# Kernel tuning notes

Measured on AMD Instinct MI355X. Metric: run time of the kernel, lower is better.

The kernel has to match this reference:

```python
import jax, jax.numpy as jnp
import numpy as np

NUM_EXP = 4  # 1 shared expert + (NUM_EXP-1) routed experts


def _mobius_add(x, y, c):
    # Mobius addition in the Poincare ball with curvature c
    x2 = jnp.sum(x * x, axis=-1, keepdims=True)
    y2 = jnp.sum(y * y, axis=-1, keepdims=True)
    xy = jnp.sum(x * y, axis=-1, keepdims=True)
    num = (1.0 + 2.0 * c * xy + c * y2) * x + (1.0 - c * x2) * y
    den = 1.0 + 2.0 * c * xy + c * c * x2 * y2
    return num / den


def _expmap(ref, v, c):
    # exponential map from tangent space at ref, curvature c (matches torch expmap)
    ref2 = jnp.sum(ref * ref, axis=-1, keepdims=True)
    sf = 2.0 / (1.0 + c * ref2)                      # scaling_factor(ref, c)
    vn = jnp.sqrt(jnp.sum(v * v, axis=-1, keepdims=True))
    second = (1.0 / jnp.sqrt(c)) * jnp.tanh(jnp.sqrt(c * sf * vn * vn / 2.0)) * (v / vn)
    return _mobius_add(ref, second, c)


def setup_inputs() -> dict:
    key = jax.random.key(0)
    ks = jax.random.split(key, 10)
    B, T, C = 2, 2048, 256
    E, H, G = 32, 4 * C, 31  # experts, ffn hidden, gate outputs (n_experts-1)
    s = 0.02
    return {
        "x": jax.random.normal(ks[0], (B, T, C), jnp.float32),
        "reference_point": jax.random.normal(ks[1], (B, T, C), jnp.float32),
        "Wg": jax.random.normal(ks[2], (C, G), jnp.float32) * s,
        "bg": jnp.zeros((G,), jnp.float32),
        "expert_bias": jnp.zeros((G,), jnp.float32),  # requires_grad=False in torch
        "Wfc": jax.random.normal(ks[3], (E, C, H), jnp.float32) * s,
        "bfc": jnp.zeros((E, H), jnp.float32),
        "Wproj": jax.random.normal(ks[4], (E, H, C), jnp.float32) * s,
        "bproj": jnp.zeros((E, C), jnp.float32),
        "c": jnp.array([0.5], jnp.float32),  # curvature param (torch.rand(1))
    }


def reference(x, reference_point, Wg, bg, expert_bias, Wfc, bfc, Wproj, bproj, c):
    b, t, C = x.shape
    n = b * t
    E = Wfc.shape[0]
    xf = x.reshape(n, C)
    rf = reference_point.reshape(n, C)

    # gate: Linear -> (noise is identity in eval) -> softmax
    gate = jax.nn.softmax(xf @ Wg + bg, axis=-1)          # [n, E-1]
    biased = gate + expert_bias
    gv, gi = jax.lax.top_k(biased, NUM_EXP - 1)            # [n, 3]
    gv = gv / jnp.sum(gv, axis=-1, keepdims=True)
    shared_w = jnp.full((n, 1), 1.0 / NUM_EXP, dtype=x.dtype)
    gate_vals = jnp.concatenate([shared_w, gv * (NUM_EXP - 1) / NUM_EXP], axis=-1)  # [n, 4]
    gate_idx = jnp.concatenate([jnp.zeros((n, 1), gi.dtype), gi + 1], axis=-1)       # [n, 4]

    # dense all-expert MLP (dropout identity in eval): [E, n, H] -> [E, n, C]
    h = jax.nn.gelu(jnp.einsum('nc,ech->enh', xf, Wfc) + bfc[:, None, :], approximate=False)
    y = jnp.einsum('enh,ehc->enc', h, Wproj) + bproj[:, None, :]
    expert_out = _expmap(rf[None, :, :], y, c)             # [E, n, C]

    # scatter_add routing weights -> [n, E]
    rw = jnp.zeros((n, E), x.dtype).at[jnp.arange(n)[:, None], gate_idx].add(gate_vals)

    out = jnp.einsum('enc,ne->nc', expert_out, rw)
    return out.reshape(b, t, C), rw
```

## Files before the change

kernel.cpp:

```cpp
#include <hip/hip_runtime.h>
#include <math.h>

#define N_TOK 4096
#define C_DIM 256
#define G_DIM 31
#define E_DIM 32
#define H_DIM 1024
#define TT    16
#define MT    32
#define TBL_MAX 576
#define NWT   (E_DIM * 64)

typedef unsigned short ushort_t;
typedef unsigned int uint_t;
typedef __attribute__((ext_vector_type(8))) short bfrag;
typedef __attribute__((ext_vector_type(4))) float f32x4;
typedef __attribute__((ext_vector_type(8))) unsigned short ushort8;

__device__ __forceinline__ ushort_t f2bf(float f) {
    uint_t u = __float_as_uint(f);
    uint_t r = (u + 0x7fffu + ((u >> 16) & 1u)) >> 16;
    return (ushort_t)r;
}

__device__ __forceinline__ float gelu_f(float v) {
    float u = 0.7978845608f * fmaf(0.044715f * v * v, v, v);
    float t = __expf(-2.f * u);
    return 0.5f * v * (1.f + (1.f - t) / (1.f + t));
}

__global__ __launch_bounds__(256) void prep_kernel(
    const float* __restrict__ Wfc, const float* __restrict__ Wproj,
    ushort_t* __restrict__ WfcF, ushort_t* __restrict__ WprojF,
    const float* __restrict__ xf, const float* __restrict__ rfp,
    const float* __restrict__ Wg, const float* __restrict__ bg,
    const float* __restrict__ ebias,
    float* __restrict__ rw_out, int* __restrict__ btok,
    float* __restrict__ bwgt, float* __restrict__ ref2_out,
    float4* __restrict__ choice, int* __restrict__ counts, int nwt)
{
    __shared__ __align__(16) char smem[36864];
    const int tid = threadIdx.x;

    if ((int)blockIdx.x < nwt) {
        ushort_t (*s)[260] = (ushort_t(*)[260])smem;
        const int b = blockIdx.x;
        const int e = b >> 6, sub = b & 63;
        const bool isfc = sub < 32;
        const float* src;
        int stride, fbbase;
        if (isfc) {
            int kt = sub >> 2, q = sub & 3;
            src = Wfc + ((size_t)e << 18) + (size_t)(kt * 32) * H_DIM + q * 256;
            stride = H_DIM;
            fbbase = e * 512 + kt * 64 + q * 16;
        } else {
            int kt = sub - 32;
            src = Wproj + ((size_t)e << 18) + (size_t)(kt * 32) * C_DIM;
            stride = C_DIM;
            fbbase = e * 512 + kt * 16;
        }
        ushort_t* dst = isfc ? WfcF : WprojF;

        float4 v[8];
        #pragma unroll
        for (int i = 0; i < 8; ++i) {
            int flat = i * 256 + tid;
            int r = flat >> 6, q4 = flat & 63;
            v[i] = *(const float4*)(src + (size_t)r * stride + q4 * 4);
        }
        #pragma unroll
        for (int i = 0; i < 8; ++i) {
            int flat = i * 256 + tid;
            int r = flat >> 6, q4 = flat & 63;
            s[r][q4 * 4 + 0] = f2bf(v[i].x);
            s[r][q4 * 4 + 1] = f2bf(v[i].y);
            s[r][q4 * 4 + 2] = f2bf(v[i].z);
            s[r][q4 * 4 + 3] = f2bf(v[i].w);
        }
        __syncthreads();

        const int l = tid & 63, w = tid >> 6;
        #pragma unroll
        for (int t = 0; t < 4; ++t) {
            int nt = w + t * 4;
            ushort8 pv;
            #pragma unroll
            for (int j = 0; j < 8; ++j)
                pv[j] = s[(l >> 4) * 8 + j][nt * 16 + (l & 15)];
            *(ushort8*)(dst + ((size_t)(fbbase + nt) * 64 + l) * 8) = pv;
        }
        return;
    }

    float* wgS = (float*)smem;
    float (*xs)[C_DIM] = (float(*)[C_DIM])(smem + 31744);
    const int b2 = blockIdx.x - nwt;
    const int w = tid >> 6, l = tid & 63;
    const int tok = b2 * 4 + w;

    if (b2 == 0 && tid == 0) counts[0] = N_TOK;

    for (int i = tid; i < C_DIM * G_DIM; i += 256) wgS[i] = Wg[i];

    float4 xv = *(const float4*)(xf + (size_t)tok * C_DIM + l * 4);
    float4 rv = *(const float4*)(rfp + (size_t)tok * C_DIM + l * 4);
    *(float4*)(&xs[w][l * 4]) = xv;
    float r2 = rv.x * rv.x + rv.y * rv.y + rv.z * rv.z + rv.w * rv.w;
    #pragma unroll
    for (int off = 32; off; off >>= 1) r2 += __shfl_xor(r2, off);
    if (l == 0) ref2_out[tok] = r2;
    __syncthreads();

    const int g = l & 31, half = l >> 5;
    float acc = 0.f;
    if (g < G_DIM) {
        const float* xr = xs[w] + half * 128;
        const float* wg = wgS + (size_t)(half * 128) * G_DIM + g;
        #pragma unroll 8
        for (int c = 0; c < 128; ++c)
            acc = fmaf(xr[c], wg[(size_t)c * G_DIM], acc);
    }
    acc += __shfl_xor(acc, 32);
    float lg = acc + ((g < G_DIM) ? bg[g] : 0.f);

    float v = (l < G_DIM) ? lg : -1e30f;
    float m = v;
    #pragma unroll
    for (int off = 32; off; off >>= 1) m = fmaxf(m, __shfl_xor(m, off));
    float pex = (l < G_DIM) ? __expf(v - m) : 0.f;
    float s = pex;
    #pragma unroll
    for (int off = 32; off; off >>= 1) s += __shfl_xor(s, off);
    float p = (l < G_DIM) ? (pex / s + ebias[l]) : -1e30f;

    float w3[3]; int id3[3];
    float vv = p;
    #pragma unroll
    for (int t = 0; t < 3; ++t) {
        float bv = vv; int bi = l;
        #pragma unroll
        for (int off = 32; off; off >>= 1) {
            float ov = __shfl_xor(bv, off); int oi = __shfl_xor(bi, off);
            if (ov > bv || (ov == bv && oi < bi)) { bv = ov; bi = oi; }
        }
        w3[t] = bv; id3[t] = bi;
        if (l == bi) vv = -1e30f;
    }
    float vs = w3[0] + w3[1] + w3[2];
    #pragma unroll
    for (int t = 0; t < 3; ++t) w3[t] = (w3[t] / vs) * 0.75f;

    if (l < 32) {
        float r = (l == 0) ? 0.25f : 0.f;
        #pragma unroll
        for (int t = 0; t < 3; ++t) if (l == id3[t] + 1) r = w3[t];
        rw_out[(size_t)tok * E_DIM + l] = r;
    }

    if (l == 0) {
        btok[tok] = tok;
        bwgt[tok] = 0.25f;
        int packed = (id3[0] + 1) | ((id3[1] + 1) << 8) | ((id3[2] + 1) << 16);
        float4 ch;
        ch.x = w3[0]; ch.y = w3[1]; ch.z = w3[2]; ch.w = __int_as_float(packed);
        choice[tok] = ch;
    }
}

__global__ __launch_bounds__(256) void bucketize_kernel(
    const float4* __restrict__ choice, int* __restrict__ btok,
    float* __restrict__ bwgt, int* __restrict__ counts,
    int* __restrict__ done, int* __restrict__ tbl)
{
    const int e = blockIdx.x + 1;
    const int tid = threadIdx.x;
    const int l = tid & 63, w = tid >> 6;
    __shared__ int wsum[4];

    int base = 0;
    for (int chunk = 0; chunk < N_TOK; chunk += 256) {
        int tok = chunk + tid;
        float4 ch = choice[tok];
        int eids = __float_as_int(ch.w);
        int m = 0; float wv = 0.f;
        if ((eids & 255) == e)              { m = 1; wv = ch.x; }
        else if (((eids >> 8) & 255) == e)  { m = 2; wv = ch.y; }
        else if (((eids >> 16) & 255) == e) { m = 3; wv = ch.z; }
        int x = m ? 1 : 0;
        #pragma unroll
        for (int off = 1; off < 64; off <<= 1) {
            int y = __shfl_up(x, off);
            if (l >= off) x += y;
        }
        if (l == 63) wsum[w] = x;
        __syncthreads();
        int waveoff = 0;
        #pragma unroll
        for (int i = 0; i < 4; ++i) if (i < w) waveoff += wsum[i];
        int total = wsum[0] + wsum[1] + wsum[2] + wsum[3];
        if (m) {
            int pos = base + waveoff + x - 1;
            btok[(size_t)e * N_TOK + pos] = tok | (m << 12);
            bwgt[(size_t)e * N_TOK + pos] = wv;
        }
        base += total;
        __syncthreads();
    }
    if (tid == 0) {
        counts[e] = base;
        if (tbl != nullptr) {
            __threadfence();
            int v = atomicAdd(done, 1);
            if (v == G_DIM - 1) {
                __threadfence();
                int tot = 0;
                for (int ee = 0; ee < E_DIM; ++ee) {
                    int cnt = counts[ee];
                    int tiles = (cnt + MT - 1) / MT;
                    for (int t = 0; t < tiles; ++t)
                        tbl[1 + tot + t] = ee | (t << 8);
                    tot += tiles;
                }
                tbl[0] = tot;
            }
        }
    }
}

__global__ __launch_bounds__(256, 2) void expert_mfma32p(
    const float* __restrict__ xf, const float* __restrict__ rfp,
    const ushort_t* __restrict__ WfcF, const ushort_t* __restrict__ WprojF,
    const float* __restrict__ bfc, const float* __restrict__ bproj,
    const float* __restrict__ cptr, const float* __restrict__ ref2p,
    const int* __restrict__ counts, const int* __restrict__ btok,
    const float* __restrict__ bwgt, const int* __restrict__ tbl,
    float* __restrict__ part)
{
    const int T = (blockIdx.x & 7) * (TBL_MAX / 8) + (blockIdx.x >> 3);
    const int tot = tbl[0];
    if (T >= tot) return;
    const int ent = tbl[1 + T];
    const int e = ent & 0xFF;
    const int base = (ent >> 8) * MT;
    const int cnt = counts[e];
    const int ntk = min(MT, cnt - base);
    const int tid = threadIdx.x;
    const int lane = tid & 63;
    const int w = tid >> 6;

    __shared__ __align__(16) ushort_t hfrag[MT * H_DIM];
    __shared__ int   spk[MT];
    __shared__ float swgt[MT];

    if (tid < MT) {
        bool vld = (base + tid) < cnt;
        spk[tid]  = btok[(size_t)e * N_TOK + (vld ? base + tid : base)];
        swgt[tid] = vld ? bwgt[(size_t)e * N_TOK + base + tid] : 0.f;
    }
    __syncthreads();

    {
        const int r  = tid >> 3;
        const int c0 = (tid & 7) * 32;
        const int mt = r >> 4, rr = r & 15;
        const int kt = c0 >> 5;
        const bool valid = (r < ntk);
        const float* xrow = xf + (size_t)(spk[r] & 0xFFF) * C_DIM;
        #pragma unroll
        for (int q = 0; q < 4; ++q) {
            ushort8 pv;
            #pragma unroll
            for (int j = 0; j < 8; ++j)
                pv[j] = f2bf(valid ? xrow[c0 + q * 8 + j] : 0.f);
            *(ushort8*)(hfrag + (size_t)((mt * 8 + kt) * 64 + (rr + 16 * q)) * 8) = pv;
        }
    }
    __syncthreads();

    bfrag afr[2][8];
    #pragma unroll
    for (int mt = 0; mt < 2; ++mt)
        #pragma unroll
        for (int kt = 0; kt < 8; ++kt)
            afr[mt][kt] = *(const bfrag*)(hfrag + (size_t)((mt * 8 + kt) * 64 + lane) * 8);
    __syncthreads();

    {
        const ushort_t* wb = WfcF + (size_t)e * 512 * 512;
        auto ldB = [&](bfrag* dst, int n1) {
            int nt = w * 16 + n1;
            #pragma unroll
            for (int kt = 0; kt < 8; ++kt)
                dst[kt] = *(const bfrag*)(wb + (size_t)(kt * 64 + nt) * 512 + lane * 8);
        };
        auto wback = [&](const f32x4& a0, const f32x4& a1, int hcol) {
            const int jj = hcol & 7, grp = (hcol & 31) >> 3, kth = hcol >> 5;
            const int rb = (lane >> 4) * 4;
            #pragma unroll
            for (int r = 0; r < 4; ++r) {
                int lp = rb + r + 16 * grp;
                hfrag[(size_t)(kth * 64 + lp) * 8 + jj]        = f2bf(gelu_f(a0[r]));
                hfrag[(size_t)((32 + kth) * 64 + lp) * 8 + jj] = f2bf(gelu_f(a1[r]));
            }
        };
        bfrag bA[8], bB[8];
        ldB(bA, 0);
        ldB(bB, 1);
        #pragma unroll 1
        for (int n1 = 0; n1 < 16; n1 += 2) {
            {
                const int hcol = (w * 16 + n1) * 16 + (lane & 15);
                const float bv = bfc[e * H_DIM + hcol];
                f32x4 a0 = {bv, bv, bv, bv}, a1 = {bv, bv, bv, bv};
                #pragma unroll
                for (int kt = 0; kt < 8; ++kt) {
                    a0 = __builtin_amdgcn_mfma_f32_16x16x32_bf16(afr[0][kt], bA[kt], a0, 0, 0, 0);
                    a1 = __builtin_amdgcn_mfma_f32_16x16x32_bf16(afr[1][kt], bA[kt], a1, 0, 0, 0);
                }
                if (n1 + 2 < 16) ldB(bA, n1 + 2);
                wback(a0, a1, hcol);
            }
            {
                const int hcol = (w * 16 + n1 + 1) * 16 + (lane & 15);
                const float bv = bfc[e * H_DIM + hcol];
                f32x4 a0 = {bv, bv, bv, bv}, a1 = {bv, bv, bv, bv};
                #pragma unroll
                for (int kt = 0; kt < 8; ++kt) {
                    a0 = __builtin_amdgcn_mfma_f32_16x16x32_bf16(afr[0][kt], bB[kt], a0, 0, 0, 0);
                    a1 = __builtin_amdgcn_mfma_f32_16x16x32_bf16(afr[1][kt], bB[kt], a1, 0, 0, 0);
                }
                if (n1 + 3 < 16) ldB(bB, n1 + 3);
                wback(a0, a1, hcol);
            }
        }
    }
    __syncthreads();

    f32x4 yac[2][4];
    #pragma unroll
    for (int mt = 0; mt < 2; ++mt)
        #pragma unroll
        for (int q = 0; q < 4; ++q) {
            int ccol = (w * 4 + q) * 16 + (lane & 15);
            float bv = bproj[e * C_DIM + ccol];
            yac[mt][q] = {bv, bv, bv, bv};
        }
    {
        const ushort_t* wb = WprojF + (size_t)e * 512 * 512;
        auto ldBp = [&](bfrag* dst, int kt) {
            #pragma unroll
            for (int q = 0; q < 4; ++q)
                dst[q] = *(const bfrag*)(wb + (size_t)(kt * 16 + w * 4 + q) * 512 + lane * 8);
        };
        auto ldAp = [&](bfrag* dst, int kt) {
            dst[0] = *(const bfrag*)(hfrag + (size_t)(kt * 64 + lane) * 8);
            dst[1] = *(const bfrag*)(hfrag + (size_t)((32 + kt) * 64 + lane) * 8);
        };
        bfrag bA[4], bB[4], aA[2], aB[2];
        ldAp(aA, 0); ldBp(bA, 0);
        ldAp(aB, 1); ldBp(bB, 1);
        #pragma unroll 1
        for (int kt = 0; kt < 32; kt += 2) {
            #pragma unroll
            for (int q = 0; q < 4; ++q) {
                yac[0][q] = __builtin_amdgcn_mfma_f32_16x16x32_bf16(aA[0], bA[q], yac[0][q], 0, 0, 0);
                yac[1][q] = __builtin_amdgcn_mfma_f32_16x16x32_bf16(aA[1], bA[q], yac[1][q], 0, 0, 0);
            }
            if (kt + 2 < 32) { ldBp(bA, kt + 2); ldAp(aA, kt + 2); }
            #pragma unroll
            for (int q = 0; q < 4; ++q) {
                yac[0][q] = __builtin_amdgcn_mfma_f32_16x16x32_bf16(aB[0], bB[q], yac[0][q], 0, 0, 0);
                yac[1][q] = __builtin_amdgcn_mfma_f32_16x16x32_bf16(aB[1], bB[q], yac[1][q], 0, 0, 0);
            }
            if (kt + 3 < 32) { ldBp(bB, kt + 3); ldAp(aB, kt + 3); }
        }
    }
    __syncthreads();

    float* ynat = (float*)hfrag;
    #pragma unroll
    for (int mt = 0; mt < 2; ++mt)
        #pragma unroll
        for (int q = 0; q < 4; ++q) {
            int ccol = (w * 4 + q) * 16 + (lane & 15);
            #pragma unroll
            for (int r = 0; r < 4; ++r) {
                int tt = mt * 16 + (lane >> 4) * 4 + r;
                ynat[tt * 260 + ccol] = yac[mt][q][r];
            }
        }
    __syncthreads();

    {
        const float cc0 = cptr[0];
        const float rsqc = sqrtf(cc0);
        #pragma unroll 1
        for (int i = 0; i < 8; ++i) {
            int tt = w * 8 + i;
            if (tt >= ntk) break;
            int pk = spk[tt];
            int tok = pk & 0xFFF, slot = pk >> 12;
            float4 yv = *(const float4*)(ynat + tt * 260 + lane * 4);
            float4 rv = *(const float4*)(rfp + (size_t)tok * C_DIM + lane * 4);
            float s2  = yv.x * yv.x + yv.y * yv.y + yv.z * yv.z + yv.w * yv.w;
            float sxy = rv.x * yv.x + rv.y * yv.y + rv.z * yv.z + rv.w * yv.w;
            #pragma unroll
            for (int off = 32; off; off >>= 1) {
                s2  += __shfl_xor(s2, off);
                sxy += __shfl_xor(sxy, off);
            }
            float ref2 = ref2p[tok];
            float sf = 2.f / (1.f + cc0 * ref2);
            float vn = sqrtf(s2);
            float aa = sqrtf(cc0 * sf * 0.5f);
            float alpha = (vn > 1e-20f) ? (tanhf(aa * vn) / (vn * rsqc)) : (aa / rsqc);
            float axy = alpha * sxy;
            float ay2 = alpha * alpha * s2;
            float A   = 1.f + 2.f * cc0 * axy + cc0 * ay2;
            float Bc  = (1.f - cc0 * ref2) * alpha;
            float den = 1.f + 2.f * cc0 * axy + cc0 * cc0 * ref2 * ay2;
            float wi  = swgt[tt] / den;
            float aco = A * wi, bco = Bc * wi;
            float4 o;
            o.x = fmaf(aco, rv.x, bco * yv.x);
            o.y = fmaf(aco, rv.y, bco * yv.y);
            o.z = fmaf(aco, rv.z, bco * yv.z);
            o.w = fmaf(aco, rv.w, bco * yv.w);
            *(float4*)(part + ((size_t)slot * N_TOK + tok) * C_DIM + lane * 4) = o;
        }
    }
}

__global__ __launch_bounds__(256) void combine_kernel(
    const float* __restrict__ part, float* __restrict__ out)
{
    const size_t NC = (size_t)N_TOK * C_DIM;
    size_t i = ((size_t)blockIdx.x * 256 + threadIdx.x) * 4;
    float4 a = *(const float4*)(part + i);
    float4 b = *(const float4*)(part + i + NC);
    float4 c = *(const float4*)(part + i + 2 * NC);
    float4 d = *(const float4*)(part + i + 3 * NC);
    float4 o;
    o.x = (a.x + b.x) + (c.x + d.x);
    o.y = (a.y + b.y) + (c.y + d.y);
    o.z = (a.z + b.z) + (c.z + d.z);
    o.w = (a.w + b.w) + (c.w + d.w);
    *(float4*)(out + i) = o;
}

__global__ __launch_bounds__(256) void expert_kernel(
    const float* __restrict__ xf, const float* __restrict__ rfp,
    const float* __restrict__ Wfc, const float* __restrict__ bfc,
    const float* __restrict__ Wproj, const float* __restrict__ bproj,
    const float* __restrict__ cptr, const float* __restrict__ ref2p,
    const int* __restrict__ counts, const int* __restrict__ btok,
    const float* __restrict__ bwgt, float* __restrict__ out)
{
    const int e = blockIdx.x;
    const int cnt = counts[e];
    const int base = blockIdx.y * TT;
    if (base >= cnt) return;
    const int nt = min(TT, cnt - base);
    const int j = threadIdx.x;

    __shared__ __align__(16) float xs[TT * C_DIM];
    __shared__ __align__(16) float hs[TT * C_DIM];
    __shared__ int   stok[TT];
    __shared__ float swgt[TT];
    __shared__ float scA[TT], scB[TT];

    if (j < nt) {
        stok[j] = btok[(size_t)e * N_TOK + base + j] & 0xFFF;
        swgt[j] = bwgt[(size_t)e * N_TOK + base + j];
    }
    __syncthreads();
    for (int t = 0; t < nt; ++t) xs[t * C_DIM + j] = xf[(size_t)stok[t] * C_DIM + j];
    for (int t = nt; t < TT; ++t) xs[t * C_DIM + j] = 0.f;
    __syncthreads();

    const float* Wfc_e = Wfc + (size_t)e * C_DIM * H_DIM;
    float h[4][TT];
    {
        float bk[4];
        #pragma unroll
        for (int k = 0; k < 4; ++k) bk[k] = bfc[(size_t)e * H_DIM + j + k * 256];
        #pragma unroll
        for (int k = 0; k < 4; ++k)
            #pragma unroll
            for (int tt = 0; tt < TT; ++tt) h[k][tt] = bk[k];
    }
    for (int c0 = 0; c0 < C_DIM; c0 += 4) {
        float wv[4][4];
        #pragma unroll
        for (int ci = 0; ci < 4; ++ci) {
            const float* wp = Wfc_e + (size_t)(c0 + ci) * H_DIM + j;
            wv[ci][0] = wp[0]; wv[ci][1] = wp[256]; wv[ci][2] = wp[512]; wv[ci][3] = wp[768];
        }
        #pragma unroll
        for (int tt = 0; tt < TT; ++tt) {
            float4 xv = *(const float4*)(xs + tt * C_DIM + c0);
            #pragma unroll
            for (int k = 0; k < 4; ++k)
                h[k][tt] += xv.x * wv[0][k] + xv.y * wv[1][k] + xv.z * wv[2][k] + xv.w * wv[3][k];
        }
    }
    #pragma unroll
    for (int k = 0; k < 4; ++k)
        #pragma unroll
        for (int tt = 0; tt < TT; ++tt) {
            float v = h[k][tt];
            h[k][tt] = 0.5f * v * (1.f + erff(v * 0.70710678118f));
        }

    const float* Wp_e = Wproj + (size_t)e * H_DIM * C_DIM;
    float yacc[TT];
    {
        float bp = bproj[(size_t)e * C_DIM + j];
        #pragma unroll
        for (int tt = 0; tt < TT; ++tt) yacc[tt] = bp;
    }
    #pragma unroll
    for (int k = 0; k < 4; ++k) {
        __syncthreads();
        #pragma unroll
        for (int tt = 0; tt < TT; ++tt) hs[tt * C_DIM + j] = h[k][tt];
        __syncthreads();
        for (int h0 = 0; h0 < 256; h0 += 4) {
            float wv[4];
            #pragma unroll
            for (int hi = 0; hi < 4; ++hi)
                wv[hi] = Wp_e[(size_t)(k * 256 + h0 + hi) * C_DIM + j];
            #pragma unroll
            for (int tt = 0; tt < TT; ++tt) {
                float4 hv = *(const float4*)(hs + tt * C_DIM + h0);
                yacc[tt] += hv.x * wv[0] + hv.y * wv[1] + hv.z * wv[2] + hv.w * wv[3];
            }
        }
    }

    __syncthreads();
    #pragma unroll
    for (int tt = 0; tt < TT; ++tt) hs[tt * C_DIM + j] = yacc[tt];
    __syncthreads();

    const float cc0 = cptr[0];
    const int wave = j >> 6, lane = j & 63;
    for (int q = 0; q < 4; ++q) {
        int tt = wave * 4 + q;
        if (tt >= nt) break;
        int tok = stok[tt];
        float s2 = 0.f, sxy = 0.f;
        #pragma unroll
        for (int m = 0; m < 4; ++m) {
            int ccol = lane + 64 * m;
            float yv = hs[tt * C_DIM + ccol];
            float rv = rfp[(size_t)tok * C_DIM + ccol];
            s2 += yv * yv; sxy += rv * yv;
        }
        #pragma unroll
        for (int off = 32; off; off >>= 1) {
            s2  += __shfl_down(s2, off);
            sxy += __shfl_down(sxy, off);
        }
        if (lane == 0) {
            float ref2 = ref2p[tok];
            float sf = 2.f / (1.f + cc0 * ref2);
            float vn = sqrtf(s2);
            float a = sqrtf(cc0 * sf * 0.5f);
            float alpha = (vn > 1e-20f)
                        ? (tanhf(a * vn) / (vn * sqrtf(cc0)))
                        : (a / sqrtf(cc0));
            float axy = alpha * sxy;
            float ay2 = alpha * alpha * s2;
            float A   = 1.f + 2.f * cc0 * axy + cc0 * ay2;
            float Bc  = (1.f - cc0 * ref2) * alpha;
            float den = 1.f + 2.f * cc0 * axy + cc0 * cc0 * ref2 * ay2;
            float wi  = swgt[tt] / den;
            scA[tt] = A * wi;
            scB[tt] = Bc * wi;
        }
    }
    __syncthreads();

    for (int tt = 0; tt < nt; ++tt) {
        int tok = stok[tt];
        float rv = rfp[(size_t)tok * C_DIM + j];
        float yv = hs[tt * C_DIM + j];
        atomicAdd(&out[(size_t)tok * C_DIM + j], scA[tt] * rv + scB[tt] * yv);
    }
}

extern "C" void kernel_launch(void* const* d_in, const int* in_sizes, int n_in,
                              void* d_out, int out_size, void* d_ws, size_t ws_size,
                              hipStream_t stream) {
    (void)in_sizes; (void)n_in; (void)out_size;
    const float* x     = (const float*)d_in[0];
    const float* rfp   = (const float*)d_in[1];
    const float* Wg    = (const float*)d_in[2];
    const float* bg    = (const float*)d_in[3];
    const float* ebias = (const float*)d_in[4];
    const float* Wfc   = (const float*)d_in[5];
    const float* bfc   = (const float*)d_in[6];
    const float* Wproj = (const float*)d_in[7];
    const float* bproj = (const float*)d_in[8];
    const float* cptr  = (const float*)d_in[9];

    float* out = (float*)d_out;
    float* rw  = out + (size_t)N_TOK * C_DIM;

    constexpr size_t OFF_DONE  = 128;
    constexpr size_t OFF_BTOK  = 256;
    constexpr size_t OFF_BWGT  = OFF_BTOK + (size_t)E_DIM * N_TOK * 4;
    constexpr size_t OFF_REF2  = OFF_BWGT + (size_t)E_DIM * N_TOK * 4;
    constexpr size_t OFF_CHO   = ((OFF_REF2 + (size_t)N_TOK * 4 + 255) / 256) * 256;
    constexpr size_t OFF_TBL   = OFF_CHO + (size_t)N_TOK * 16;
    constexpr size_t OFF_WFC   = OFF_TBL + 4096;
    constexpr size_t SZ_W      = (size_t)E_DIM * C_DIM * H_DIM * 2;
    constexpr size_t OFF_WPROJ = OFF_WFC + SZ_W;
    constexpr size_t OFF_PART  = OFF_WPROJ + SZ_W;
    constexpr size_t SZ_PART   = (size_t)4 * N_TOK * C_DIM * 4;
    constexpr size_t WS_FULL   = OFF_PART + SZ_PART;

    char*  ws     = (char*)d_ws;
    int*   counts = (int*)ws;
    int*   done   = (int*)(ws + OFF_DONE);
    int*   btok   = (int*)(ws + OFF_BTOK);
    float* bwgt   = (float*)(ws + OFF_BWGT);
    float* ref2   = (float*)(ws + OFF_REF2);
    float4* cho   = (float4*)(ws + OFF_CHO);
    int*   tbl    = (int*)(ws + OFF_TBL);

    hipMemsetAsync(ws, 0, 256, stream);

    if (ws_size >= WS_FULL) {
        ushort_t* WfcF   = (ushort_t*)(ws + OFF_WFC);
        ushort_t* WprojF = (ushort_t*)(ws + OFF_WPROJ);
        float*    part   = (float*)(ws + OFF_PART);
        prep_kernel<<<NWT + 1024, 256, 0, stream>>>(
            Wfc, Wproj, WfcF, WprojF, x, rfp, Wg, bg, ebias,
            rw, btok, bwgt, ref2, cho, counts, NWT);
        bucketize_kernel<<<G_DIM, 256, 0, stream>>>(cho, btok, bwgt, counts, done, tbl);
        expert_mfma32p<<<TBL_MAX, 256, 0, stream>>>(x, rfp, WfcF, WprojF, bfc, bproj,
                                                    cptr, ref2, counts, btok, bwgt, tbl, part);
        combine_kernel<<<(N_TOK * C_DIM) / 1024, 256, 0, stream>>>(part, out);
    } else {
        hipMemsetAsync(out, 0, (size_t)N_TOK * C_DIM * sizeof(float), stream);
        prep_kernel<<<1024, 256, 0, stream>>>(
            Wfc, Wproj, nullptr, nullptr, x, rfp, Wg, bg, ebias,
            rw, btok, bwgt, ref2, cho, counts, 0);
        bucketize_kernel<<<G_DIM, 256, 0, stream>>>(cho, btok, bwgt, counts, done, nullptr);
        dim3 grid(E_DIM, N_TOK / TT);
        expert_kernel<<<grid, 256, 0, stream>>>(x, rfp, Wfc, bfc, Wproj, bproj,
                                                cptr, ref2, counts, btok, bwgt, out);
    }
}
```

Before: 141.7 us.

## Chunk expert hidden dimension to halve LDS and split prep into two kernels

The expert kernel now processes the 1024-wide hidden layer in two 512-column chunks. Each chunk runs the FC GEMM plus GELU into a half-size LDS buffer and then accumulates its share of the projection GEMM. This cuts shared memory from 64KB to about 33KB and raises the launch-bounds occupancy target from 2 to 4 blocks per CU. The combined prep kernel is split into separate weight-transpose and gate kernels, which adds a launch and extra barriers but removes the branch and shared-memory sizing coupling. Raising the occupancy target may also constrain register allocation.

```diff
diff --git a/kernel.cpp b/kernel.cpp
--- a/kernel.cpp
+++ b/kernel.cpp
@@ -9,7 +9,6 @@
 #define TT    16
 #define MT    32
 #define TBL_MAX 576
-#define NWT   (E_DIM * 64)
 
 typedef unsigned short ushort_t;
 typedef unsigned int uint_t;
@@ -29,77 +28,75 @@
     return 0.5f * v * (1.f + (1.f - t) / (1.f + t));
 }
 
-__global__ __launch_bounds__(256) void prep_kernel(
+__global__ __launch_bounds__(256) void wtrans_kernel(
     const float* __restrict__ Wfc, const float* __restrict__ Wproj,
-    ushort_t* __restrict__ WfcF, ushort_t* __restrict__ WprojF,
+    ushort_t* __restrict__ WfcF, ushort_t* __restrict__ WprojF)
+{
+    __shared__ __align__(16) ushort_t s[32][260];
+    const int tid = threadIdx.x;
+    const int b = blockIdx.x;
+    const int e = b >> 6, sub = b & 63;
+    const bool isfc = sub < 32;
+    const float* src;
+    int stride, fbbase;
+    if (isfc) {
+        int kt = sub >> 2, q = sub & 3;
+        src = Wfc + ((size_t)e << 18) + (size_t)(kt * 32) * H_DIM + q * 256;
+        stride = H_DIM;
+        fbbase = e * 512 + kt * 64 + q * 16;
+    } else {
+        int kt = sub - 32;
+        src = Wproj + ((size_t)e << 18) + (size_t)(kt * 32) * C_DIM;
+        stride = C_DIM;
+        fbbase = e * 512 + kt * 16;
+    }
+    ushort_t* dst = isfc ? WfcF : WprojF;
+
+    float4 v[8];
+    #pragma unroll
+    for (int i = 0; i < 8; ++i) {
+        int flat = i * 256 + tid;
+        int r = flat >> 6, q4 = flat & 63;
+        v[i] = *(const float4*)(src + (size_t)r * stride + q4 * 4);
+    }
+    #pragma unroll
+    for (int i = 0; i < 8; ++i) {
+        int flat = i * 256 + tid;
+        int r = flat >> 6, q4 = flat & 63;
+        s[r][q4 * 4 + 0] = f2bf(v[i].x);
+        s[r][q4 * 4 + 1] = f2bf(v[i].y);
+        s[r][q4 * 4 + 2] = f2bf(v[i].z);
+        s[r][q4 * 4 + 3] = f2bf(v[i].w);
+    }
+    __syncthreads();
+
+    const int l = tid & 63, w = tid >> 6;
+    #pragma unroll
+    for (int t = 0; t < 4; ++t) {
+        int nt = w + t * 4;
+        ushort8 pv;
+        #pragma unroll
+        for (int j = 0; j < 8; ++j)
+            pv[j] = s[(l >> 4) * 8 + j][nt * 16 + (l & 15)];
+        *(ushort8*)(dst + ((size_t)(fbbase + nt) * 64 + l) * 8) = pv;
+    }
+}
+
+__global__ __launch_bounds__(256) void gate_kernel(
     const float* __restrict__ xf, const float* __restrict__ rfp,
     const float* __restrict__ Wg, const float* __restrict__ bg,
     const float* __restrict__ ebias,
     float* __restrict__ rw_out, int* __restrict__ btok,
     float* __restrict__ bwgt, float* __restrict__ ref2_out,
-    float4* __restrict__ choice, int* __restrict__ counts, int nwt)
+    float4* __restrict__ choice, int* __restrict__ counts)
 {
-    __shared__ __align__(16) char smem[36864];
+    __shared__ float wgS[C_DIM * G_DIM];
+    __shared__ __align__(16) float xs[4][C_DIM];
     const int tid = threadIdx.x;
-
-    if ((int)blockIdx.x < nwt) {
-        ushort_t (*s)[260] = (ushort_t(*)[260])smem;
-        const int b = blockIdx.x;
-        const int e = b >> 6, sub = b & 63;
-        const bool isfc = sub < 32;
-        const float* src;
-        int stride, fbbase;
-        if (isfc) {
-            int kt = sub >> 2, q = sub & 3;
-            src = Wfc + ((size_t)e << 18) + (size_t)(kt * 32) * H_DIM + q * 256;
-            stride = H_DIM;
-            fbbase = e * 512 + kt * 64 + q * 16;
-        } else {
-            int kt = sub - 32;
-            src = Wproj + ((size_t)e << 18) + (size_t)(kt * 32) * C_DIM;
-            stride = C_DIM;
-            fbbase = e * 512 + kt * 16;
-        }
-        ushort_t* dst = isfc ? WfcF : WprojF;
-
-        float4 v[8];
-        #pragma unroll
-        for (int i = 0; i < 8; ++i) {
-            int flat = i * 256 + tid;
-            int r = flat >> 6, q4 = flat & 63;
-            v[i] = *(const float4*)(src + (size_t)r * stride + q4 * 4);
-        }
-        #pragma unroll
-        for (int i = 0; i < 8; ++i) {
-            int flat = i * 256 + tid;
-            int r = flat >> 6, q4 = flat & 63;
-            s[r][q4 * 4 + 0] = f2bf(v[i].x);
-            s[r][q4 * 4 + 1] = f2bf(v[i].y);
-            s[r][q4 * 4 + 2] = f2bf(v[i].z);
-            s[r][q4 * 4 + 3] = f2bf(v[i].w);
-        }
-        __syncthreads();
-
-        const int l = tid & 63, w = tid >> 6;
-        #pragma unroll
-        for (int t = 0; t < 4; ++t) {
-            int nt = w + t * 4;
-            ushort8 pv;
-            #pragma unroll
-            for (int j = 0; j < 8; ++j)
-                pv[j] = s[(l >> 4) * 8 + j][nt * 16 + (l & 15)];
-            *(ushort8*)(dst + ((size_t)(fbbase + nt) * 64 + l) * 8) = pv;
-        }
-        return;
-    }
-
-    float* wgS = (float*)smem;
-    float (*xs)[C_DIM] = (float(*)[C_DIM])(smem + 31744);
-    const int b2 = blockIdx.x - nwt;
     const int w = tid >> 6, l = tid & 63;
-    const int tok = b2 * 4 + w;
-
-    if (b2 == 0 && tid == 0) counts[0] = N_TOK;
+    const int tok = blockIdx.x * 4 + w;
+
+    if (blockIdx.x == 0 && tid == 0) counts[0] = N_TOK;
 
     for (int i = tid; i < C_DIM * G_DIM; i += 256) wgS[i] = Wg[i];
 
@@ -228,7 +225,7 @@
     }
 }
 
-__global__ __launch_bounds__(256, 2) void expert_mfma32p(
+__global__ __launch_bounds__(256, 4) void expert_mfma32hc(
     const float* __restrict__ xf, const float* __restrict__ rfp,
     const ushort_t* __restrict__ WfcF, const ushort_t* __restrict__ WprojF,
     const float* __restrict__ bfc, const float* __restrict__ bproj,
@@ -249,7 +246,8 @@
     const int lane = tid & 63;
     const int w = tid >> 6;
 
-    __shared__ __align__(16) ushort_t hfrag[MT * H_DIM];
+    __shared__ __align__(16) char smem[33792];
+    ushort_t* hbuf = (ushort_t*)smem;
     __shared__ int   spk[MT];
     __shared__ float swgt[MT];
 
@@ -273,7 +271,7 @@
             #pragma unroll
             for (int j = 0; j < 8; ++j)
                 pv[j] = f2bf(valid ? xrow[c0 + q * 8 + j] : 0.f);
-            *(ushort8*)(hfrag + (size_t)((mt * 8 + kt) * 64 + (rr + 16 * q)) * 8) = pv;
+            *(ushort8*)(hbuf + (size_t)((mt * 8 + kt) * 64 + (rr + 16 * q)) * 8) = pv;
         }
     }
     __syncthreads();
@@ -283,58 +281,7 @@
     for (int mt = 0; mt < 2; ++mt)
         #pragma unroll
         for (int kt = 0; kt < 8; ++kt)
-            afr[mt][kt] = *(const bfrag*)(hfrag + (size_t)((mt * 8 + kt) * 64 + lane) * 8);
-    __syncthreads();
-
-    {
-        const ushort_t* wb = WfcF + (size_t)e * 512 * 512;
-        auto ldB = [&](bfrag* dst, int n1) {
-            int nt = w * 16 + n1;
-            #pragma unroll
-            for (int kt = 0; kt < 8; ++kt)
-                dst[kt] = *(const bfrag*)(wb + (size_t)(kt * 64 + nt) * 512 + lane * 8);
-        };
-        auto wback = [&](const f32x4& a0, const f32x4& a1, int hcol) {
-            const int jj = hcol & 7, grp = (hcol & 31) >> 3, kth = hcol >> 5;
-            const int rb = (lane >> 4) * 4;
-            #pragma unroll
-            for (int r = 0; r < 4; ++r) {
-                int lp = rb + r + 16 * grp;
-                hfrag[(size_t)(kth * 64 + lp) * 8 + jj]        = f2bf(gelu_f(a0[r]));
-                hfrag[(size_t)((32 + kth) * 64 + lp) * 8 + jj] = f2bf(gelu_f(a1[r]));
-            }
-        };
-        bfrag bA[8], bB[8];
-        ldB(bA, 0);
-        ldB(bB, 1);
-        #pragma unroll 1
-        for (int n1 = 0; n1 < 16; n1 += 2) {
-            {
-                const int hcol = (w * 16 + n1) * 16 + (lane & 15);
-                const float bv = bfc[e * H_DIM + hcol];
-                f32x4 a0 = {bv, bv, bv, bv}, a1 = {bv, bv, bv, bv};
-                #pragma unroll
-                for (int kt = 0; kt < 8; ++kt) {
-                    a0 = __builtin_amdgcn_mfma_f32_16x16x32_bf16(afr[0][kt], bA[kt], a0, 0, 0, 0);
-                    a1 = __builtin_amdgcn_mfma_f32_16x16x32_bf16(afr[1][kt], bA[kt], a1, 0, 0, 0);
-                }
-                if (n1 + 2 < 16) ldB(bA, n1 + 2);
-                wback(a0, a1, hcol);
-            }
-            {
-                const int hcol = (w * 16 + n1 + 1) * 16 + (lane & 15);
-                const float bv = bfc[e * H_DIM + hcol];
-                f32x4 a0 = {bv, bv, bv, bv}, a1 = {bv, bv, bv, bv};
-                #pragma unroll
-                for (int kt = 0; kt < 8; ++kt) {
-                    a0 = __builtin_amdgcn_mfma_f32_16x16x32_bf16(afr[0][kt], bB[kt], a0, 0, 0, 0);
-                    a1 = __builtin_amdgcn_mfma_f32_16x16x32_bf16(afr[1][kt], bB[kt], a1, 0, 0, 0);
-                }
-                if (n1 + 3 < 16) ldB(bB, n1 + 3);
-                wback(a0, a1, hcol);
-            }
-        }
-    }
+            afr[mt][kt] = *(const bfrag*)(hbuf + (size_t)((mt * 8 + kt) * 64 + lane) * 8);
     __syncthreads();
 
     f32x4 yac[2][4];
@@ -346,39 +293,98 @@
             float bv = bproj[e * C_DIM + ccol];
             yac[mt][q] = {bv, bv, bv, bv};
         }
-    {
-        const ushort_t* wb = WprojF + (size_t)e * 512 * 512;
-        auto ldBp = [&](bfrag* dst, int kt) {
-            #pragma unroll
-            for (int q = 0; q < 4; ++q)
-                dst[q] = *(const bfrag*)(wb + (size_t)(kt * 16 + w * 4 + q) * 512 + lane * 8);
-        };
-        auto ldAp = [&](bfrag* dst, int kt) {
-            dst[0] = *(const bfrag*)(hfrag + (size_t)(kt * 64 + lane) * 8);
-            dst[1] = *(const bfrag*)(hfrag + (size_t)((32 + kt) * 64 + lane) * 8);
-        };
-        bfrag bA[4], bB[4], aA[2], aB[2];
-        ldAp(aA, 0); ldBp(bA, 0);
-        ldAp(aB, 1); ldBp(bB, 1);
-        #pragma unroll 1
-        for (int kt = 0; kt < 32; kt += 2) {
-            #pragma unroll
-            for (int q = 0; q < 4; ++q) {
-                yac[0][q] = __builtin_amdgcn_mfma_f32_16x16x32_bf16(aA[0], bA[q], yac[0][q], 0, 0, 0);
-                yac[1][q] = __builtin_amdgcn_mfma_f32_16x16x32_bf16(aA[1], bA[q], yac[1][q], 0, 0, 0);
+
+    const ushort_t* wbf = WfcF + (size_t)e * 512 * 512;
+    const ushort_t* wbp = WprojF + (size_t)e * 512 * 512;
+
+    #pragma unroll 1
+    for (int c = 0; c < 2; ++c) {
+        {
+            auto ldB = [&](bfrag* dst, int n1) {
+                int nt = c * 32 + w * 8 + n1;
+                #pragma unroll
+                for (int kt = 0; kt < 8; ++kt)
+                    dst[kt] = *(const bfrag*)(wbf + (size_t)(kt * 64 + nt) * 512 + lane * 8);
+            };
+            auto wback = [&](const f32x4& a0, const f32x4& a1, int nt) {
+                const int hcol = nt * 16 + (lane & 15);
+                const int cc = hcol - c * 512;
+                const int jj = cc & 7, grp = (cc & 31) >> 3, kth = cc >> 5;
+                const int rb = (lane >> 4) * 4;
+                #pragma unroll
+                for (int r = 0; r < 4; ++r) {
+                    int lp = rb + r + 16 * grp;
+                    hbuf[(size_t)(kth * 64 + lp) * 8 + jj]        = f2bf(gelu_f(a0[r]));
+                    hbuf[(size_t)((16 + kth) * 64 + lp) * 8 + jj] = f2bf(gelu_f(a1[r]));
+                }
+            };
+            bfrag bA[8], bB[8];
+            ldB(bA, 0);
+            ldB(bB, 1);
+            #pragma unroll 1
+            for (int n1 = 0; n1 < 8; n1 += 2) {
+                {
+                    const int nt = c * 32 + w * 8 + n1;
+                    const float bv = bfc[e * H_DIM + nt * 16 + (lane & 15)];
+                    f32x4 a0 = {bv, bv, bv, bv}, a1 = {bv, bv, bv, bv};
+                    #pragma unroll
+                    for (int kt = 0; kt < 8; ++kt) {
+                        a0 = __builtin_amdgcn_mfma_f32_16x16x32_bf16(afr[0][kt], bA[kt], a0, 0, 0, 0);
+                        a1 = __builtin_amdgcn_mfma_f32_16x16x32_bf16(afr[1][kt], bA[kt], a1, 0, 0, 0);
+                    }
+                    if (n1 + 2 < 8) ldB(bA, n1 + 2);
+                    wback(a0, a1, nt);
+                }
+                {
+                    const int nt = c * 32 + w * 8 + n1 + 1;
+                    const float bv = bfc[e * H_DIM + nt * 16 + (lane & 15)];
+                    f32x4 a0 = {bv, bv, bv, bv}, a1 = {bv, bv, bv, bv};
+                    #pragma unroll
+                    for (int kt = 0; kt < 8; ++kt) {
+                        a0 = __builtin_amdgcn_mfma_f32_16x16x32_bf16(afr[0][kt], bB[kt], a0, 0, 0, 0);
+                        a1 = __builtin_amdgcn_mfma_f32_16x16x32_bf16(afr[1][kt], bB[kt], a1, 0, 0, 0);
+                    }
+                    if (n1 + 3 < 8) ldB(bB, n1 + 3);
+                    wback(a0, a1, nt);
+                }
             }
-            if (kt + 2 < 32) { ldBp(bA, kt + 2); ldAp(aA, kt + 2); }
-            #pragma unroll
-            for (int q = 0; q < 4; ++q) {
-                yac[0][q] = __builtin_amdgcn_mfma_f32_16x16x32_bf16(aB[0], bB[q], yac[0][q], 0, 0, 0);
-                yac[1][q] = __builtin_amdgcn_mfma_f32_16x16x32_bf16(aB[1], bB[q], yac[1][q], 0, 0, 0);
+        }
+        __syncthreads();
+
+        {
+            auto ldBp = [&](bfrag* dst, int ktl) {
+                int ktg = c * 16 + ktl;
+                #pragma unroll
+                for (int q = 0; q < 4; ++q)
+                    dst[q] = *(const bfrag*)(wbp + (size_t)(ktg * 16 + w * 4 + q) * 512 + lane * 8);
+            };
+            auto ldAp = [&](bfrag* dst, int ktl) {
+                dst[0] = *(const bfrag*)(hbuf + (size_t)(ktl * 64 + lane) * 8);
+                dst[1] = *(const bfrag*)(hbuf + (size_t)((16 + ktl) * 64 + lane) * 8);
+            };
+            bfrag bA[4], bB[4], aA[2], aB[2];
+            ldAp(aA, 0); ldBp(bA, 0);
+            ldAp(aB, 1); ldBp(bB, 1);
+            #pragma unroll 1
+            for (int ktl = 0; ktl < 16; ktl += 2) {
+                #pragma unroll
+                for (int q = 0; q < 4; ++q) {
+                    yac[0][q] = __builtin_amdgcn_mfma_f32_16x16x32_bf16(aA[0], bA[q], yac[0][q], 0, 0, 0);
+                    yac[1][q] = __builtin_amdgcn_mfma_f32_16x16x32_bf16(aA[1], bA[q], yac[1][q], 0, 0, 0);
+                }
+                if (ktl + 2 < 16) { ldBp(bA, ktl + 2); ldAp(aA, ktl + 2); }
+                #pragma unroll
+                for (int q = 0; q < 4; ++q) {
+                    yac[0][q] = __builtin_amdgcn_mfma_f32_16x16x32_bf16(aB[0], bB[q], yac[0][q], 0, 0, 0);
+                    yac[1][q] = __builtin_amdgcn_mfma_f32_16x16x32_bf16(aB[1], bB[q], yac[1][q], 0, 0, 0);
+                }
+                if (ktl + 3 < 16) { ldBp(bB, ktl + 3); ldAp(aB, ktl + 3); }
             }
-            if (kt + 3 < 32) { ldBp(bB, kt + 3); ldAp(aB, kt + 3); }
-        }
-    }
-    __syncthreads();
-
-    float* ynat = (float*)hfrag;
+        }
+        __syncthreads();
+    }
+
+    float* ynat = (float*)smem;
     #pragma unroll
     for (int mt = 0; mt < 2; ++mt)
         #pragma unroll
@@ -387,7 +393,7 @@
             #pragma unroll
             for (int r = 0; r < 4; ++r) {
                 int tt = mt * 16 + (lane >> 4) * 4 + r;
-                ynat[tt * 260 + ccol] = yac[mt][q][r];
+                ynat[tt * 264 + ccol] = yac[mt][q][r];
             }
         }
     __syncthreads();
@@ -401,7 +407,7 @@
             if (tt >= ntk) break;
             int pk = spk[tt];
             int tok = pk & 0xFFF, slot = pk >> 12;
-            float4 yv = *(const float4*)(ynat + tt * 260 + lane * 4);
+            float4 yv = *(const float4*)(ynat + tt * 264 + lane * 4);
             float4 rv = *(const float4*)(rfp + (size_t)tok * C_DIM + lane * 4);
             float s2  = yv.x * yv.x + yv.y * yv.y + yv.z * yv.z + yv.w * yv.w;
             float sxy = rv.x * yv.x + rv.y * yv.y + rv.z * yv.z + rv.w * yv.w;
@@ -637,18 +643,17 @@
         ushort_t* WfcF   = (ushort_t*)(ws + OFF_WFC);
         ushort_t* WprojF = (ushort_t*)(ws + OFF_WPROJ);
         float*    part   = (float*)(ws + OFF_PART);
-        prep_kernel<<<NWT + 1024, 256, 0, stream>>>(
-            Wfc, Wproj, WfcF, WprojF, x, rfp, Wg, bg, ebias,
-            rw, btok, bwgt, ref2, cho, counts, NWT);
+        wtrans_kernel<<<E_DIM * 64, 256, 0, stream>>>(Wfc, Wproj, WfcF, WprojF);
+        gate_kernel<<<N_TOK / 4, 256, 0, stream>>>(x, rfp, Wg, bg, ebias,
+                                                   rw, btok, bwgt, ref2, cho, counts);
         bucketize_kernel<<<G_DIM, 256, 0, stream>>>(cho, btok, bwgt, counts, done, tbl);
-        expert_mfma32p<<<TBL_MAX, 256, 0, stream>>>(x, rfp, WfcF, WprojF, bfc, bproj,
-                                                    cptr, ref2, counts, btok, bwgt, tbl, part);
+        expert_mfma32hc<<<TBL_MAX, 256, 0, stream>>>(x, rfp, WfcF, WprojF, bfc, bproj,
+                                                     cptr, ref2, counts, btok, bwgt, tbl, part);
         combine_kernel<<<(N_TOK * C_DIM) / 1024, 256, 0, stream>>>(part, out);
     } else {
         hipMemsetAsync(out, 0, (size_t)N_TOK * C_DIM * sizeof(float), stream);
-        prep_kernel<<<1024, 256, 0, stream>>>(
-            Wfc, Wproj, nullptr, nullptr, x, rfp, Wg, bg, ebias,
-            rw, btok, bwgt, ref2, cho, counts, 0);
+        gate_kernel<<<N_TOK / 4, 256, 0, stream>>>(x, rfp, Wg, bg, ebias,
+                                                   rw, btok, bwgt, ref2, cho, counts);
         bucketize_kernel<<<G_DIM, 256, 0, stream>>>(cho, btok, bwgt, counts, done, nullptr);
         dim3 grid(E_DIM, N_TOK / TT);
         expert_kernel<<<grid, 256, 0, stream>>>(x, rfp, Wfc, bfc, Wproj, bproj,
```

Measured after the change: 213.7 us. 1.51x slower.
